# Kernel tuning notes

Measured on AMD Instinct MI355X. Metric: run time of the kernel, lower is better.

## Reference

```python
import jax, jax.numpy as jnp
import numpy as np

N_LAYERS = 4
GAMMA = 0.5
D_MODEL = 256
D_STATE = 64
D_CONV = 4
EXPAND = 2
D_INNER = EXPAND * D_MODEL            # 512 (= headdim, so nheads = 1)
NHEADS = 1
CONV_DIM = D_INNER + 2 * D_STATE      # 640
D_IN_PROJ = 2 * D_INNER + 2 * D_STATE + NHEADS  # 1153
VOCAB = 100
VOCAB_PAD = 104                        # padded to multiple of 8 by MambaConfig
BATCH = 8
SEQ = 2048


def setup_inputs() -> dict:
    key = jax.random.key(0)
    ks = jax.random.split(key, 8)
    def nrm(k, shape):
        # gamma init: std = 1 / d1**gamma, d1 = shape[0]
        return (jax.random.normal(k, shape, jnp.float32) * (1.0 / shape[0] ** GAMMA))
    inp = {}
    inp["input_ids"] = jax.random.randint(ks[0], (BATCH, SEQ), 0, VOCAB)
    inp["embed"] = nrm(ks[1], (VOCAB_PAD, D_MODEL))          # tied embedding / lm_head
    inp["in_proj_w"] = nrm(ks[2], (N_LAYERS * D_IN_PROJ, D_MODEL)).reshape(N_LAYERS, D_IN_PROJ, D_MODEL)
    inp["conv_w"] = nrm(ks[3], (N_LAYERS * CONV_DIM, D_CONV)).reshape(N_LAYERS, CONV_DIM, D_CONV)
    inp["conv_b"] = jnp.zeros((N_LAYERS, CONV_DIM), jnp.float32)
    inp["dt_bias"] = jax.random.uniform(ks[4], (N_LAYERS, NHEADS), jnp.float32, -4.0, -1.0)
    inp["A_log"] = jnp.log(jax.random.uniform(ks[5], (N_LAYERS, NHEADS), jnp.float32, 1.0, 16.0))
    inp["Dparam"] = jnp.ones((N_LAYERS, NHEADS), jnp.float32)
    inp["norm_g_w"] = jnp.ones((N_LAYERS, D_INNER), jnp.float32)
    inp["out_proj_w"] = nrm(ks[6], (N_LAYERS * D_MODEL, D_INNER)).reshape(N_LAYERS, D_MODEL, D_INNER)
    inp["block_norm_w"] = jnp.ones((N_LAYERS, D_MODEL), jnp.float32)
    inp["norm_f_w"] = jnp.ones((D_MODEL,), jnp.float32)
    return inp


def rmsnorm(x, w, eps=1e-5):
    return x * jax.lax.rsqrt(jnp.mean(x * x, axis=-1, keepdims=True) + eps) * w


def ssm_scan(x, dt, A, Bc, Cc):
    # x: (B,L,P)  dt: (B,L)  A: scalar  Bc,Cc: (B,L,N). Sequential selective scan.
    def step(h, inp):  # h: (B,P,N)
        x_t, dt_t, b_t, c_t = inp
        h = h * jnp.exp(dt_t * A)[:, None, None] + (dt_t[:, None] * x_t)[:, :, None] * b_t[:, None, :]
        y = jnp.einsum('bpn,bn->bp', h, c_t)
        return h, y
    h0 = jnp.zeros((x.shape[0], x.shape[2], Bc.shape[2]), x.dtype)
    xs = (jnp.swapaxes(x, 0, 1), jnp.swapaxes(dt, 0, 1), jnp.swapaxes(Bc, 0, 1), jnp.swapaxes(Cc, 0, 1))
    _, ys = jax.lax.scan(step, h0, xs)
    return jnp.swapaxes(ys, 0, 1)  # (B,L,P)


def mamba2_mixer(h, ipw, cw, cb, dtb, alog, dp, ngw, opw):
    zxbcdt = h @ ipw.T                                   # (B,L,1153)
    z = zxbcdt[..., :D_INNER]
    xBC = zxbcdt[..., D_INNER:D_INNER + CONV_DIM]
    dt_raw = zxbcdt[..., D_INNER + CONV_DIM:]            # (B,L,1)
    # depthwise causal conv1d (kernel D_CONV) + SiLU
    xp = jnp.pad(xBC, ((0, 0), (D_CONV - 1, 0), (0, 0)))
    L = xBC.shape[1]
    conv = sum(xp[:, k:k + L, :] * cw[:, k] for k in range(D_CONV)) + cb
    xBC = jax.nn.silu(conv)
    x = xBC[..., :D_INNER]
    Bc = xBC[..., D_INNER:D_INNER + D_STATE]
    Cc = xBC[..., D_INNER + D_STATE:]
    dt = jax.nn.softplus(dt_raw[..., 0] + dtb[0])        # (B,L), nheads=1
    A = -jnp.exp(alog[0])
    y = ssm_scan(x, dt, A, Bc, Cc) + dp[0] * x
    y = rmsnorm(y * jax.nn.silu(z), ngw)                 # RMSNormGated (norm after gate)
    return y @ opw.T


def reference(input_ids, embed, in_proj_w, conv_w, conv_b, dt_bias, A_log, Dparam,
              norm_g_w, out_proj_w, block_norm_w, norm_f_w):
    hidden = embed[input_ids]                            # (B,L,D_MODEL)
    residual = None
    for i in range(N_LAYERS):
        residual = hidden if residual is None else hidden + residual
        hidden = rmsnorm(residual, block_norm_w[i])
        hidden = mamba2_mixer(hidden, in_proj_w[i], conv_w[i], conv_b[i], dt_bias[i],
                              A_log[i], Dparam[i], norm_g_w[i], out_proj_w[i])
    residual = hidden + residual
    final = rmsnorm(residual, norm_f_w)
    logits = final @ embed.T                             # tied lm_head, (B,L,VOCAB_PAD)
    return logits[:, -1, :VOCAB]                         # last-token logits, (B,VOCAB)
```

## Files before the change

kernel.cpp:

```cpp
#include <hip/hip_runtime.h>
#include <math.h>

#define NB    8
#define LSEQ  2048
#define TKN   16384
#define DM    256
#define DI    512
#define DS    64
#define DIP   1153
#define DIPP  1160
#define CDIM  640
#define NL    4
#define NC    16
#define CL    128
#define VOC   100

typedef short bf16x8 __attribute__((ext_vector_type(8)));
typedef short bf16x4 __attribute__((ext_vector_type(4)));
typedef float f32x4  __attribute__((ext_vector_type(4)));
typedef unsigned short ushort_t;

__device__ __forceinline__ float block_reduce_sum256(float v) {
  __shared__ float sred[4];
  #pragma unroll
  for (int off = 32; off > 0; off >>= 1) v += __shfl_down(v, off, 64);
  int lane = threadIdx.x & 63, wid = threadIdx.x >> 6;
  if (lane == 0) sred[wid] = v;
  __syncthreads();
  return sred[0] + sred[1] + sred[2] + sred[3];
}

__device__ __forceinline__ unsigned short f2bf(float f) {
  unsigned int u = __float_as_uint(f);
  unsigned int r = u + 0x7FFFu + ((u >> 16) & 1u);
  return (unsigned short)(r >> 16);
}
__device__ __forceinline__ float bf2f(unsigned short u) {
  return __uint_as_float(((unsigned int)u) << 16);
}

__global__ __launch_bounds__(256) void convert_w(const float* __restrict__ ipw,
    const float* __restrict__ opw, ushort_t* __restrict__ wbi, ushort_t* __restrict__ wbo) {
  const int n1 = NL * DIP * DM;
  const int n2 = NL * DM * DI;
  int i4 = (blockIdx.x * 256 + threadIdx.x) * 4;
  if (i4 < n1) {
    float4 v = *(const float4*)(ipw + i4);
    bf16x4 o; o[0] = (short)f2bf(v.x); o[1] = (short)f2bf(v.y);
    o[2] = (short)f2bf(v.z); o[3] = (short)f2bf(v.w);
    *(bf16x4*)(wbi + i4) = o;
  } else {
    int j = i4 - n1;
    if (j < n2) {
      float4 v = *(const float4*)(opw + j);
      bf16x4 o; o[0] = (short)f2bf(v.x); o[1] = (short)f2bf(v.y);
      o[2] = (short)f2bf(v.z); o[3] = (short)f2bf(v.w);
      *(bf16x4*)(wbo + j) = o;
    }
  }
}

__global__ __launch_bounds__(256) void add_rmsnorm(float* __restrict__ resid,
    const float* __restrict__ mixo, ushort_t* __restrict__ hn, const float* __restrict__ w,
    const int* __restrict__ ids, const float* __restrict__ embed, int first) {
  int wave = threadIdx.x >> 6, lane = threadIdx.x & 63;
  int t = blockIdx.x * 4 + wave;
  size_t o = (size_t)t * DM + lane * 4;
  float4 r4;
  if (first) {
    int id = ids[t];
    r4 = *(const float4*)&embed[(size_t)id * DM + lane * 4];
  } else {
    float4 m4 = *(const float4*)&mixo[o];
    r4 = *(const float4*)&resid[o];
    r4.x += m4.x; r4.y += m4.y; r4.z += m4.z; r4.w += m4.w;
  }
  *(float4*)&resid[o] = r4;
  float ss = r4.x * r4.x + r4.y * r4.y + r4.z * r4.z + r4.w * r4.w;
  #pragma unroll
  for (int m = 32; m >= 1; m >>= 1) ss += __shfl_xor(ss, m, 64);
  float sc = rsqrtf(ss * (1.f / DM) + 1e-5f);
  float4 w4 = *(const float4*)&w[lane * 4];
  bf16x4 o4;
  o4[0] = (short)f2bf(r4.x * sc * w4.x);
  o4[1] = (short)f2bf(r4.y * sc * w4.y);
  o4[2] = (short)f2bf(r4.z * sc * w4.z);
  o4[3] = (short)f2bf(r4.w * sc * w4.w);
  *(bf16x4*)&hn[o] = o4;
}

#define LSTR  40
#define LSTR2 72
template<typename TC>
__global__ __launch_bounds__(256) void gemm_nt_bf16(const ushort_t* __restrict__ A,
    const ushort_t* __restrict__ Bw, TC* __restrict__ C, int N, int K, int ldc) {
  __shared__ short sA[128 * LSTR2];
  __shared__ short sB[128 * LSTR2];
  int tid = threadIdx.x;
  int bn = blockIdx.x * 128;
  int bm = blockIdx.y * 128;
  int wave = tid >> 6, lane = tid & 63;
  int wm = (wave >> 1) * 64, wn = (wave & 1) * 64;
  int q = lane >> 4, c = lane & 15;

  f32x4 acc[4][4];
  #pragma unroll
  for (int i = 0; i < 4; ++i)
    #pragma unroll
    for (int j = 0; j < 4; ++j) acc[i][j] = (f32x4)0.f;

  int sr = tid >> 1;
  int sc = (tid & 1) * 32;
  const ushort_t* Ag = A + (size_t)(bm + sr) * K + sc;
  const ushort_t* Bg = Bw + (size_t)(bn + sr) * K + sc;
  bool bok = (bn + sr) < N;
  short* sAp = &sA[sr * LSTR2 + sc];
  short* sBp = &sB[sr * LSTR2 + sc];

  for (int k0 = 0; k0 < K; k0 += 64) {
    bf16x8 a0 = *(const bf16x8*)(Ag + k0);
    bf16x8 a1 = *(const bf16x8*)(Ag + k0 + 8);
    bf16x8 a2 = *(const bf16x8*)(Ag + k0 + 16);
    bf16x8 a3 = *(const bf16x8*)(Ag + k0 + 24);
    bf16x8 b0 = (bf16x8)(short)0, b1 = (bf16x8)(short)0;
    bf16x8 b2 = (bf16x8)(short)0, b3 = (bf16x8)(short)0;
    if (bok) {
      b0 = *(const bf16x8*)(Bg + k0);
      b1 = *(const bf16x8*)(Bg + k0 + 8);
      b2 = *(const bf16x8*)(Bg + k0 + 16);
      b3 = *(const bf16x8*)(Bg + k0 + 24);
    }
    __syncthreads();
    *(bf16x8*)(sAp)      = a0;
    *(bf16x8*)(sAp + 8)  = a1;
    *(bf16x8*)(sAp + 16) = a2;
    *(bf16x8*)(sAp + 24) = a3;
    *(bf16x8*)(sBp)      = b0;
    *(bf16x8*)(sBp + 8)  = b1;
    *(bf16x8*)(sBp + 16) = b2;
    *(bf16x8*)(sBp + 24) = b3;
    __syncthreads();
    #pragma unroll
    for (int ks = 0; ks < 2; ++ks) {
      bf16x8 af[4], bfr[4];
      #pragma unroll
      for (int i = 0; i < 4; ++i)
        af[i] = *(const bf16x8*)&sA[(wm + i * 16 + c) * LSTR2 + ks * 32 + q * 8];
      #pragma unroll
      for (int j = 0; j < 4; ++j)
        bfr[j] = *(const bf16x8*)&sB[(wn + j * 16 + c) * LSTR2 + ks * 32 + q * 8];
      #pragma unroll
      for (int i = 0; i < 4; ++i)
        #pragma unroll
        for (int j = 0; j < 4; ++j)
          acc[i][j] = __builtin_amdgcn_mfma_f32_16x16x32_bf16(af[i], bfr[j], acc[i][j], 0, 0, 0);
    }
  }
  #pragma unroll
  for (int i = 0; i < 4; ++i) {
    int m = bm + wm + i * 16 + q * 4;
    #pragma unroll
    for (int j = 0; j < 4; ++j) {
      int n = bn + wn + j * 16 + c;
      if (n < N) {
        #pragma unroll
        for (int r = 0; r < 4; ++r) {
          if constexpr (sizeof(TC) == 2)
            C[(size_t)(m + r) * ldc + n] = (TC)f2bf(acc[i][j][r]);
          else
            C[(size_t)(m + r) * ldc + n] = acc[i][j][r];
        }
      }
    }
  }
}

__global__ __launch_bounds__(256) void outproj_fused(const ushort_t* __restrict__ yb,
    const ushort_t* __restrict__ zx, const ushort_t* __restrict__ Bw,
    const float* __restrict__ gw, float* __restrict__ Cout) {
  __shared__ short sA[64 * LSTR];
  __shared__ short sB[128 * LSTR];
  __shared__ float swl[DI];
  __shared__ float rs[256];
  int tid = threadIdx.x;
  int bn = blockIdx.x * 128;
  int bm = blockIdx.y * 64;
  int wave = tid >> 6, lane = tid & 63;
  int wm = (wave >> 1) * 32, wn = (wave & 1) * 64;
  int q = lane >> 4, c = lane & 15;
  swl[tid] = gw[tid];
  swl[tid + 256] = gw[tid + 256];

  f32x4 acc[2][4];
  #pragma unroll
  for (int i = 0; i < 2; ++i)
    #pragma unroll
    for (int j = 0; j < 4; ++j) acc[i][j] = (f32x4)0.f;

  int ar = tid >> 2, ak = (tid & 3) * 8;
  int br = tid >> 1, bk = (tid & 1) * 16;
  const ushort_t* yrow = yb + (size_t)(bm + ar) * DI + ak;
  const ushort_t* zrow = zx + (size_t)(bm + ar) * DIPP + ak;
  const ushort_t* Bg = Bw + (size_t)(bn + br) * DI + bk;
  short* sAp = &sA[ar * LSTR + ak];
  short* sBp = &sB[br * LSTR + bk];
  float sumsq = 0.f;
  __syncthreads();

  for (int k0 = 0; k0 < DI; k0 += 32) {
    bf16x8 y8 = *(const bf16x8*)(yrow + k0);
    bf16x8 z8 = *(const bf16x8*)(zrow + k0);
    bf16x8 b0 = *(const bf16x8*)(Bg + k0);
    bf16x8 b1 = *(const bf16x8*)(Bg + k0 + 8);
    bf16x8 g8;
    #pragma unroll
    for (int e = 0; e < 8; ++e) {
      float zz = bf2f((ushort_t)z8[e]);
      float gg = bf2f((ushort_t)y8[e]) * (zz / (1.f + __expf(-zz)));
      sumsq += gg * gg;
      g8[e] = (short)f2bf(gg * swl[k0 + ak + e]);
    }
    __syncthreads();
    *(bf16x8*)(sAp)     = g8;
    *(bf16x8*)(sBp)     = b0;
    *(bf16x8*)(sBp + 8) = b1;
    __syncthreads();
    bf16x8 af[2], bfr[4];
    #pragma unroll
    for (int i = 0; i < 2; ++i)
      af[i] = *(const bf16x8*)&sA[(wm + i * 16 + c) * LSTR + q * 8];
    #pragma unroll
    for (int j = 0; j < 4; ++j)
      bfr[j] = *(const bf16x8*)&sB[(wn + j * 16 + c) * LSTR + q * 8];
    #pragma unroll
    for (int i = 0; i < 2; ++i)
      #pragma unroll
      for (int j = 0; j < 4; ++j)
        acc[i][j] = __builtin_amdgcn_mfma_f32_16x16x32_bf16(af[i], bfr[j], acc[i][j], 0, 0, 0);
  }
  rs[tid] = sumsq;
  __syncthreads();
  #pragma unroll
  for (int i = 0; i < 2; ++i) {
    #pragma unroll
    for (int r = 0; r < 4; ++r) {
      int ml = wm + i * 16 + q * 4 + r;
      float rtot = rs[ml * 4] + rs[ml * 4 + 1] + rs[ml * 4 + 2] + rs[ml * 4 + 3];
      float scale = rsqrtf(rtot * (1.f / DI) + 1e-5f);
      #pragma unroll
      for (int j = 0; j < 4; ++j) {
        int n = bn + wn + j * 16 + c;
        Cout[(size_t)(bm + ml) * DM + n] = scale * acc[i][j][r];
      }
    }
  }
}

__global__ __launch_bounds__(256) void conv_silu(const ushort_t* __restrict__ zx,
    const float* __restrict__ cw, const float* __restrict__ cb,
    const float* __restrict__ dtb, ushort_t* __restrict__ xo,
    ushort_t* __restrict__ Bo, ushort_t* __restrict__ Co, ushort_t* __restrict__ Ut) {
  __shared__ ushort_t tile[67 * 128];
  __shared__ ushort_t tt[128 * 72];
  __shared__ float sdt[64];
  int tid = threadIdx.x;
  int ct = blockIdx.x, tb_ = blockIdx.y, b = blockIdx.z;
  int c0 = ct * 128, l0 = tb_ * 64;
  size_t rowb = (size_t)b * LSEQ;
  bool isx = (ct < 4);
  for (int slot = tid; slot < 67 * 16; slot += 256) {
    int r = slot >> 4, gg = slot & 15;
    int l = l0 + r - 3;
    bf16x8 v = (bf16x8)(short)0;
    if (l >= 0) v = *(const bf16x8*)&zx[(rowb + l) * DIPP + DI + c0 + gg * 8];
    *(bf16x8*)&tile[r * 128 + gg * 8] = v;
  }
  if (isx && tid < 64) sdt[tid] = dtb[rowb + l0 + tid];
  int g = tid & 15, tq = tid >> 4;
  int cbase = c0 + g * 8;
  float w[4][8], bias[8];
  #pragma unroll
  for (int e = 0; e < 8; ++e) {
    float4 wv = *(const float4*)&cw[(cbase + e) * 4];
    w[0][e] = wv.x; w[1][e] = wv.y; w[2][e] = wv.z; w[3][e] = wv.w;
    bias[e] = cb[cbase + e];
  }
  __syncthreads();
  bf16x8 rows[7];
  #pragma unroll
  for (int r = 0; r < 7; ++r)
    rows[r] = *(const bf16x8*)&tile[(tq * 4 + r) * 128 + g * 8];
  #pragma unroll
  for (int it = 0; it < 4; ++it) {
    int t = tq * 4 + it;
    size_t tl = rowb + l0 + t;
    float dtv = isx ? sdt[t] : 0.f;
    bf16x8 o;
    #pragma unroll
    for (int e = 0; e < 8; ++e) {
      float s = bias[e]
              + w[0][e] * bf2f((ushort_t)rows[it][e])
              + w[1][e] * bf2f((ushort_t)rows[it + 1][e])
              + w[2][e] * bf2f((ushort_t)rows[it + 2][e])
              + w[3][e] * bf2f((ushort_t)rows[it + 3][e]);
      float v = s / (1.f + __expf(-s));
      o[e] = (short)f2bf(v);
      if (isx) tt[(g * 8 + e) * 72 + t] = f2bf(v * dtv);
    }
    if (isx) {
      *(bf16x8*)&xo[tl * DI + cbase] = o;
    } else if (g < 8) {
      *(bf16x8*)&Bo[tl * DS + (cbase - DI)] = o;
    } else {
      *(bf16x8*)&Co[tl * DS + (cbase - DI - DS)] = o;
    }
  }
  if (isx) {
    __syncthreads();
    #pragma unroll
    for (int pass = 0; pass < 4; ++pass) {
      int slot = pass * 256 + tid;
      int op = slot >> 3, sg = slot & 7;
      bf16x8 v = *(const bf16x8*)&tt[op * 72 + sg * 8];
      *(bf16x8*)&Ut[((size_t)b * DI + c0 + op) * LSEQ + l0 + sg * 8] = v;
    }
  }
}

__global__ __launch_bounds__(256) void csum_k(const ushort_t* __restrict__ zx,
    const float* __restrict__ dtbias, float* __restrict__ dtb, float* __restrict__ csumb) {
  int tid = threadIdx.x;
  int wave = tid >> 6, lane = tid & 63;
  int cg = blockIdx.x * 4 + wave;
  int b = cg >> 4, ch = cg & 15;
  size_t base = (size_t)b * LSEQ + ch * CL;
  float bias = dtbias[0];
  float x0 = bf2f(zx[(base + 2 * lane) * DIPP + (DIP - 1)]) + bias;
  float x1 = bf2f(zx[(base + 2 * lane + 1) * DIPP + (DIP - 1)]) + bias;
  float d0 = (x0 > 20.f) ? x0 : log1pf(__expf(x0));
  float d1 = (x1 > 20.f) ? x1 : log1pf(__expf(x1));
  dtb[base + 2 * lane] = d0;
  dtb[base + 2 * lane + 1] = d1;
  float p = d0 + d1;
  #pragma unroll
  for (int off = 1; off < 64; off <<= 1) {
    float t = __shfl_up(p, off, 64);
    if (lane >= off) p += t;
  }
  csumb[base + 2 * lane]     = p - d1;
  csumb[base + 2 * lane + 1] = p;
}

__global__ __launch_bounds__(256) void state_gemm(const ushort_t* __restrict__ Bb,
    const ushort_t* __restrict__ Ut, const float* __restrict__ csumb,
    const float* __restrict__ alog, float* __restrict__ hst) {
  __shared__ short sW[64 * 144];
  __shared__ short sX[128 * 40];
  __shared__ float scs[128];
  int tid = threadIdx.x;
  int ph = blockIdx.x, ch = blockIdx.y, b = blockIdx.z;
  int bc = b * NC + ch;
  size_t tb = (size_t)b * LSEQ + ch * CL;
  float Aval = -expf(alog[0]);
  if (tid < 128) scs[tid] = csumb[tb + tid];
  __syncthreads();
  float Stot = scs[127];
  {
    int s = tid >> 1, noff = (tid & 1) * 32;
    float scale = __expf(Aval * (Stot - scs[s]));
    #pragma unroll
    for (int blk = 0; blk < 4; ++blk) {
      bf16x8 v = *(const bf16x8*)&Bb[(tb + s) * DS + noff + blk * 8];
      #pragma unroll
      for (int e = 0; e < 8; ++e)
        sW[(noff + blk * 8 + e) * 144 + s] = (short)f2bf(bf2f((ushort_t)v[e]) * scale);
    }
  }
  int wave = tid >> 6, lane = tid & 63;
  int wn = (wave >> 1) * 32, wp = (wave & 1) * 64;
  int q = lane >> 4, c = lane & 15;
  f32x4 acc[2][4];
  #pragma unroll
  for (int i = 0; i < 2; ++i)
    #pragma unroll
    for (int j = 0; j < 4; ++j) acc[i][j] = (f32x4)0.f;

  for (int ks = 0; ks < 4; ++ks) {
    __syncthreads();
    {
      int r = tid >> 1, off = (tid & 1) * 16;
      size_t ua = ((size_t)b * DI + ph * 128 + r) * LSEQ + ch * CL + ks * 32 + off;
      bf16x8 u0 = *(const bf16x8*)&Ut[ua];
      bf16x8 u1 = *(const bf16x8*)&Ut[ua + 8];
      *(bf16x8*)&sX[r * 40 + off]     = u0;
      *(bf16x8*)&sX[r * 40 + off + 8] = u1;
    }
    __syncthreads();
    bf16x8 af[2], bfr[4];
    #pragma unroll
    for (int i = 0; i < 2; ++i)
      af[i] = *(const bf16x8*)&sW[(wn + i * 16 + c) * 144 + ks * 32 + q * 8];
    #pragma unroll
    for (int j = 0; j < 4; ++j)
      bfr[j] = *(const bf16x8*)&sX[(wp + j * 16 + c) * 40 + q * 8];
    #pragma unroll
    for (int i = 0; i < 2; ++i)
      #pragma unroll
      for (int j = 0; j < 4; ++j)
        acc[i][j] = __builtin_amdgcn_mfma_f32_16x16x32_bf16(af[i], bfr[j], acc[i][j], 0, 0, 0);
  }
  #pragma unroll
  for (int i = 0; i < 2; ++i) {
    int n = wn + i * 16 + q * 4;
    #pragma unroll
    for (int j = 0; j < 4; ++j) {
      int pg = ph * 128 + wp + j * 16 + c;
      #pragma unroll
      for (int r = 0; r < 4; ++r)
        hst[((size_t)bc * DS + n + r) * DI + pg] = acc[i][j][r];
    }
  }
}

__global__ __launch_bounds__(256) void combine2(const float* __restrict__ hst,
    const float* __restrict__ csumb, const float* __restrict__ alog,
    ushort_t* __restrict__ hin) {
  __shared__ ushort_t ts[64 * 17];
  int tid = threadIdx.x;
  int pt = blockIdx.x, nt = blockIdx.y, b = blockIdx.z;
  int p0 = pt * 64, n0 = nt * 16;
  int pl = tid & 63, ng = tid >> 6;
  float Aval = -expf(alog[0]);
  float h[4];
  #pragma unroll
  for (int i = 0; i < 4; ++i) h[i] = 0.f;
  for (int c = 0; c < NC; ++c) {
    int bc = b * NC + c;
    #pragma unroll
    for (int i = 0; i < 4; ++i)
      ts[pl * 17 + ng * 4 + i] = f2bf(h[i]);
    __syncthreads();
    {
      int on = tid & 15;
      #pragma unroll
      for (int pass = 0; pass < 4; ++pass) {
        int op = (tid >> 4) + pass * 16;
        hin[((size_t)bc * DI + p0 + op) * DS + n0 + on] = ts[op * 17 + on];
      }
    }
    __syncthreads();
    float Sc = csumb[(size_t)b * LSEQ + c * CL + CL - 1];
    float dec = __expf(Aval * Sc);
    #pragma unroll
    for (int i = 0; i < 4; ++i) {
      float loc = hst[((size_t)bc * DS + n0 + ng * 4 + i) * DI + p0 + pl];
      h[i] = h[i] * dec + loc;
    }
  }
}

__global__ __launch_bounds__(256) void y_gemm(const ushort_t* __restrict__ Bb,
    const ushort_t* __restrict__ Cb, const ushort_t* __restrict__ Ut,
    const ushort_t* __restrict__ hin, const float* __restrict__ csumb,
    const float* __restrict__ alog, const float* __restrict__ dpar,
    const ushort_t* __restrict__ xb, ushort_t* __restrict__ y) {
  __shared__ short sC[128 * 72];
  __shared__ short sM[128 * 136];
  __shared__ short sU[128 * 80];
  __shared__ float scs[128];
  int tid = threadIdx.x;
  int ph = blockIdx.x, ch = blockIdx.y, b = blockIdx.z;
  int bc = b * NC + ch;
  size_t tb = (size_t)b * LSEQ + ch * CL;
  float Aval = -expf(alog[0]);
  float dp = dpar[0];
  int wave = tid >> 6, lane = tid & 63;
  int q = lane >> 4, c = lane & 15;

  {
    int r = tid >> 1, off = (tid & 1) * 32;
    #pragma unroll
    for (int blk = 0; blk < 4; ++blk) {
      *(bf16x8*)&sC[r * 72 + off + blk * 8] = *(const bf16x8*)&Cb[(tb + r) * DS + off + blk * 8];
      *(bf16x8*)&sU[r * 80 + off + blk * 8] = *(const bf16x8*)&Bb[(tb + r) * DS + off + blk * 8];
    }
  }
  if (tid < 128) scs[tid] = csumb[tb + tid];
  __syncthreads();

  {
    int wm = (wave >> 1) * 64, wss = (wave & 1) * 64;
    if (wave == 1) {
      #pragma unroll
      for (int i = 0; i < 4; ++i) {
        #pragma unroll
        for (int r = 0; r < 4; ++r) {
          int t = i * 16 + q * 4 + r;
          #pragma unroll
          for (int j = 0; j < 4; ++j)
            sM[t * 136 + 64 + j * 16 + c] = 0;
        }
      }
    } else {
      f32x4 g[4][4];
      #pragma unroll
      for (int i = 0; i < 4; ++i)
        #pragma unroll
        for (int j = 0; j < 4; ++j) g[i][j] = (f32x4)0.f;
      #pragma unroll
      for (int k0 = 0; k0 < 64; k0 += 32) {
        bf16x8 af[4], bfr[4];
        #pragma unroll
        for (int i = 0; i < 4; ++i)
          af[i] = *(const bf16x8*)&sC[(wm + i * 16 + c) * 72 + k0 + q * 8];
        #pragma unroll
        for (int j = 0; j < 4; ++j)
          bfr[j] = *(const bf16x8*)&sU[(wss + j * 16 + c) * 80 + k0 + q * 8];
        #pragma unroll
        for (int i = 0; i < 4; ++i)
          #pragma unroll
          for (int j = 0; j < 4; ++j)
            g[i][j] = __builtin_amdgcn_mfma_f32_16x16x32_bf16(af[i], bfr[j], g[i][j], 0, 0, 0);
      }
      #pragma unroll
      for (int i = 0; i < 4; ++i) {
        #pragma unroll
        for (int r = 0; r < 4; ++r) {
          int t = wm + i * 16 + q * 4 + r;
          float ct = scs[t];
          #pragma unroll
          for (int j = 0; j < 4; ++j) {
            int s = wss + j * 16 + c;
            float v = g[i][j][r];
            float m = (s <= t) ? v * __expf(Aval * (ct - scs[s])) : 0.f;
            sM[t * 136 + s] = (short)f2bf(m);
          }
        }
      }
    }
  }

  int wm2 = (wave >> 1) * 64, wp = (wave & 1) * 64;
  f32x4 acc[4][4];
  #pragma unroll
  for (int i = 0; i < 4; ++i)
    #pragma unroll
    for (int j = 0; j < 4; ++j) acc[i][j] = (f32x4)0.f;

  for (int ks = 0; ks < 4; ++ks) {
    __syncthreads();
    {
      int r = tid >> 1, off = (tid & 1) * 16;
      size_t ua = ((size_t)b * DI + ph * 128 + r) * LSEQ + ch * CL + ks * 32 + off;
      bf16x8 u0 = *(const bf16x8*)&Ut[ua];
      bf16x8 u1 = *(const bf16x8*)&Ut[ua + 8];
      *(bf16x8*)&sU[r * 40 + off]     = u0;
      *(bf16x8*)&sU[r * 40 + off + 8] = u1;
    }
    __syncthreads();
    bf16x8 af[4], bfr[4];
    #pragma unroll
    for (int i = 0; i < 4; ++i)
      af[i] = *(const bf16x8*)&sM[(wm2 + i * 16 + c) * 136 + ks * 32 + q * 8];
    #pragma unroll
    for (int j = 0; j < 4; ++j)
      bfr[j] = *(const bf16x8*)&sU[(wp + j * 16 + c) * 40 + q * 8];
    #pragma unroll
    for (int i = 0; i < 4; ++i)
      #pragma unroll
      for (int j = 0; j < 4; ++j)
        acc[i][j] = __builtin_amdgcn_mfma_f32_16x16x32_bf16(af[i], bfr[j], acc[i][j], 0, 0, 0);
  }

  __syncthreads();
  {
    int r = tid >> 1, off = (tid & 1) * 32;
    float sc_t = __expf(Aval * scs[r]);
    #pragma unroll
    for (int blk = 0; blk < 4; ++blk) {
      bf16x8 v = *(const bf16x8*)&sC[r * 72 + off + blk * 8];
      bf16x8 o;
      #pragma unroll
      for (int e = 0; e < 8; ++e)
        o[e] = (short)f2bf(bf2f((ushort_t)v[e]) * sc_t);
      *(bf16x8*)&sM[r * 80 + off + blk * 8] = o;
    }
  }
  for (int ks = 4; ks < 6; ++ks) {
    __syncthreads();
    {
      int r = tid >> 1, off = (tid & 1) * 16;
      size_t ha = ((size_t)bc * DI + ph * 128 + r) * DS + (ks - 4) * 32 + off;
      bf16x8 h0 = *(const bf16x8*)&hin[ha];
      bf16x8 h1 = *(const bf16x8*)&hin[ha + 8];
      *(bf16x8*)&sU[r * 40 + off]     = h0;
      *(bf16x8*)&sU[r * 40 + off + 8] = h1;
    }
    __syncthreads();
    bf16x8 af[4], bfr[4];
    #pragma unroll
    for (int i = 0; i < 4; ++i)
      af[i] = *(const bf16x8*)&sM[(wm2 + i * 16 + c) * 80 + (ks - 4) * 32 + q * 8];
    #pragma unroll
    for (int j = 0; j < 4; ++j)
      bfr[j] = *(const bf16x8*)&sU[(wp + j * 16 + c) * 40 + q * 8];
    #pragma unroll
    for (int i = 0; i < 4; ++i)
      #pragma unroll
      for (int j = 0; j < 4; ++j)
        acc[i][j] = __builtin_amdgcn_mfma_f32_16x16x32_bf16(af[i], bfr[j], acc[i][j], 0, 0, 0);
  }

  #pragma unroll
  for (int i = 0; i < 4; ++i) {
    #pragma unroll
    for (int r = 0; r < 4; ++r) {
      int t = wm2 + i * 16 + q * 4 + r;
      size_t row = (tb + t) * DI;
      #pragma unroll
      for (int j = 0; j < 4; ++j) {
        int pg = ph * 128 + wp + j * 16 + c;
        y[row + pg] = f2bf(acc[i][j][r] + dp * bf2f(xb[row + pg]));
      }
    }
  }
}

__global__ __launch_bounds__(256) void finalize(const float* __restrict__ resid,
    const float* __restrict__ mixo, const float* __restrict__ embed,
    const float* __restrict__ nfw, float* __restrict__ out) {
  int b = blockIdx.x, tid = threadIdx.x;
  __shared__ float fin[DM];
  size_t off = ((size_t)b * LSEQ + (LSEQ - 1)) * DM;
  float r = resid[off + tid] + mixo[off + tid];
  float ss = block_reduce_sum256(r * r);
  fin[tid] = r * rsqrtf(ss * (1.f / DM) + 1e-5f) * nfw[tid];
  __syncthreads();
  if (tid < VOC) {
    float acc = 0.f;
    #pragma unroll 8
    for (int d = 0; d < DM; ++d) acc += fin[d] * embed[(size_t)tid * DM + d];
    out[b * VOC + tid] = acc;
  }
}

extern "C" void kernel_launch(void* const* d_in, const int* in_sizes, int n_in,
                              void* d_out, int out_size, void* d_ws, size_t ws_size,
                              hipStream_t stream) {
  const int*   ids   = (const int*)d_in[0];
  const float* embed = (const float*)d_in[1];
  const float* ipw   = (const float*)d_in[2];
  const float* cw    = (const float*)d_in[3];
  const float* cb    = (const float*)d_in[4];
  const float* dtbias= (const float*)d_in[5];
  const float* alog  = (const float*)d_in[6];
  const float* dpar  = (const float*)d_in[7];
  const float* ngw   = (const float*)d_in[8];
  const float* opw   = (const float*)d_in[9];
  const float* bnw   = (const float*)d_in[10];
  const float* nfw   = (const float*)d_in[11];
  float* out = (float*)d_out;

  char* p = (char*)d_ws;
  float* resid = (float*)p;            p += (size_t)TKN * DM * 4;
  float* mixo  = (float*)p;            p += (size_t)TKN * DM * 4;
  ushort_t* hn = (ushort_t*)p;         p += (size_t)TKN * DM * 2;
  ushort_t* zx = (ushort_t*)p;         p += (size_t)TKN * DIPP * 2;
  float* dtb   = (float*)p;            p += (size_t)TKN * 4;
  float* csumb = (float*)p;            p += (size_t)TKN * 4;
  ushort_t* xb = (ushort_t*)p;         p += (size_t)TKN * DI * 2;
  ushort_t* yb = (ushort_t*)p;         p += (size_t)TKN * DI * 2;
  ushort_t* Bb = (ushort_t*)p;         p += (size_t)TKN * DS * 2;
  ushort_t* Cb = (ushort_t*)p;         p += (size_t)TKN * DS * 2;
  ushort_t* Ut = (ushort_t*)p;         p += (size_t)TKN * DI * 2;
  ushort_t* hin= (ushort_t*)p;         p += (size_t)NB * NC * DI * DS * 2;
  ushort_t* wbi= (ushort_t*)p;         p += (size_t)NL * DIP * DM * 2;
  ushort_t* wbo= (ushort_t*)p;         p += (size_t)NL * DM * DI * 2;
  float* hst = (float*)yb;

  convert_w<<<(NL * DIP * DM + NL * DM * DI + 1023) / 1024, 256, 0, stream>>>(
      ipw, opw, wbi, wbo);

  for (int i = 0; i < NL; ++i) {
    add_rmsnorm<<<TKN / 4, 256, 0, stream>>>(resid, mixo, hn, bnw + (size_t)i * DM,
                                             ids, embed, i == 0 ? 1 : 0);
    gemm_nt_bf16<ushort_t><<<dim3((DIP + 127) / 128, TKN / 128), 256, 0, stream>>>(
        hn, wbi + (size_t)i * DIP * DM, zx, DIP, DM, DIPP);
    csum_k<<<32, 256, 0, stream>>>(zx, dtbias + i, dtb, csumb);
    conv_silu<<<dim3(CDIM / 128, LSEQ / 64, NB), 256, 0, stream>>>(
        zx, cw + (size_t)i * CDIM * 4, cb + (size_t)i * CDIM, dtb, xb, Bb, Cb, Ut);
    state_gemm<<<dim3(4, NC, NB), 256, 0, stream>>>(Bb, Ut, csumb, alog + i, hst);
    combine2<<<dim3(DI / 64, 4, NB), 256, 0, stream>>>(hst, csumb, alog + i, hin);
    y_gemm<<<dim3(4, NC, NB), 256, 0, stream>>>(Bb, Cb, Ut, hin, csumb, alog + i,
                                                dpar + i, xb, yb);
    outproj_fused<<<dim3(2, TKN / 64), 256, 0, stream>>>(
        yb, zx, wbo + (size_t)i * DM * DI, ngw + (size_t)i * DI, mixo);
  }

  finalize<<<NB, 256, 0, stream>>>(resid, mixo, embed, nfw, out);
}
```

Before: 580.5 us.

## Prefetch U/h tiles into registers, pack sM stores, skip zero causal MFMAs

In state_gemm and y_gemm, the next K-slice of Ut (and later hin) is loaded into registers while the current slice is computed, so global latency overlaps the MFMA work. The bf16 writes to sM are packed into 32-bit stores by pairing lanes with a shuffle. Waves whose rows lie in the first causal half skip the MFMAs for the upper-triangular K slices, which are all zero. The cost is extra register pressure and some control-flow divergence across waves.

After: 584.6 us. Within noise of the previous version (+0.7%).

```diff
diff --git a/kernel.cpp b/kernel.cpp
--- a/kernel.cpp
+++ b/kernel.cpp
@@ -362,6 +362,10 @@
   int bc = b * NC + ch;
   size_t tb = (size_t)b * LSEQ + ch * CL;
   float Aval = -expf(alog[0]);
+  int r2 = tid >> 1, off16 = (tid & 1) * 16;
+  size_t ubase = ((size_t)b * DI + ph * 128 + r2) * LSEQ + ch * CL + off16;
+  bf16x8 pf0 = *(const bf16x8*)&Ut[ubase];
+  bf16x8 pf1 = *(const bf16x8*)&Ut[ubase + 8];
   if (tid < 128) scs[tid] = csumb[tb + tid];
   __syncthreads();
   float Stot = scs[127];
@@ -387,13 +391,11 @@
 
   for (int ks = 0; ks < 4; ++ks) {
     __syncthreads();
-    {
-      int r = tid >> 1, off = (tid & 1) * 16;
-      size_t ua = ((size_t)b * DI + ph * 128 + r) * LSEQ + ch * CL + ks * 32 + off;
-      bf16x8 u0 = *(const bf16x8*)&Ut[ua];
-      bf16x8 u1 = *(const bf16x8*)&Ut[ua + 8];
-      *(bf16x8*)&sX[r * 40 + off]     = u0;
-      *(bf16x8*)&sX[r * 40 + off + 8] = u1;
+    *(bf16x8*)&sX[r2 * 40 + off16]     = pf0;
+    *(bf16x8*)&sX[r2 * 40 + off16 + 8] = pf1;
+    if (ks < 3) {
+      pf0 = *(const bf16x8*)&Ut[ubase + (ks + 1) * 32];
+      pf1 = *(const bf16x8*)&Ut[ubase + (ks + 1) * 32 + 8];
     }
     __syncthreads();
     bf16x8 af[2], bfr[4];
@@ -477,6 +479,12 @@
   int wave = tid >> 6, lane = tid & 63;
   int q = lane >> 4, c = lane & 15;
 
+  int r2 = tid >> 1, off16 = (tid & 1) * 16;
+  size_t ubase = ((size_t)b * DI + ph * 128 + r2) * LSEQ + ch * CL + off16;
+  size_t hbase = ((size_t)bc * DI + ph * 128 + r2) * DS + off16;
+  bf16x8 pf0 = *(const bf16x8*)&Ut[ubase];
+  bf16x8 pf1 = *(const bf16x8*)&Ut[ubase + 8];
+
   {
     int r = tid >> 1, off = (tid & 1) * 32;
     #pragma unroll
@@ -496,9 +504,11 @@
         #pragma unroll
         for (int r = 0; r < 4; ++r) {
           int t = i * 16 + q * 4 + r;
-          #pragma unroll
-          for (int j = 0; j < 4; ++j)
-            sM[t * 136 + 64 + j * 16 + c] = 0;
+          if ((c & 1) == 0) {
+            #pragma unroll
+            for (int j = 0; j < 4; ++j)
+              *(unsigned int*)&sM[t * 136 + 64 + j * 16 + c] = 0u;
+          }
         }
       }
     } else {
@@ -533,7 +543,10 @@
             int s = wss + j * 16 + c;
             float v = g[i][j][r];
             float m = (s <= t) ? v * __expf(Aval * (ct - scs[s])) : 0.f;
-            sM[t * 136 + s] = (short)f2bf(m);
+            unsigned int mb = (unsigned int)f2bf(m);
+            unsigned int partner = __shfl_xor(mb, 1, 64);
+            if ((c & 1) == 0)
+              *(unsigned int*)&sM[t * 136 + s] = mb | (partner << 16);
           }
         }
       }
@@ -549,27 +562,30 @@
 
   for (int ks = 0; ks < 4; ++ks) {
     __syncthreads();
-    {
-      int r = tid >> 1, off = (tid & 1) * 16;
-      size_t ua = ((size_t)b * DI + ph * 128 + r) * LSEQ + ch * CL + ks * 32 + off;
-      bf16x8 u0 = *(const bf16x8*)&Ut[ua];
-      bf16x8 u1 = *(const bf16x8*)&Ut[ua + 8];
-      *(bf16x8*)&sU[r * 40 + off]     = u0;
-      *(bf16x8*)&sU[r * 40 + off + 8] = u1;
-    }
-    __syncthreads();
-    bf16x8 af[4], bfr[4];
-    #pragma unroll
-    for (int i = 0; i < 4; ++i)
-      af[i] = *(const bf16x8*)&sM[(wm2 + i * 16 + c) * 136 + ks * 32 + q * 8];
-    #pragma unroll
-    for (int j = 0; j < 4; ++j)
-      bfr[j] = *(const bf16x8*)&sU[(wp + j * 16 + c) * 40 + q * 8];
-    #pragma unroll
-    for (int i = 0; i < 4; ++i)
+    *(bf16x8*)&sU[r2 * 40 + off16]     = pf0;
+    *(bf16x8*)&sU[r2 * 40 + off16 + 8] = pf1;
+    if (ks < 3) {
+      pf0 = *(const bf16x8*)&Ut[ubase + (ks + 1) * 32];
+      pf1 = *(const bf16x8*)&Ut[ubase + (ks + 1) * 32 + 8];
+    } else {
+      pf0 = *(const bf16x8*)&hin[hbase];
+      pf1 = *(const bf16x8*)&hin[hbase + 8];
+    }
+    __syncthreads();
+    if (!(wm2 == 0 && ks >= 2)) {
+      bf16x8 af[4], bfr[4];
+      #pragma unroll
+      for (int i = 0; i < 4; ++i)
+        af[i] = *(const bf16x8*)&sM[(wm2 + i * 16 + c) * 136 + ks * 32 + q * 8];
       #pragma unroll
       for (int j = 0; j < 4; ++j)
-        acc[i][j] = __builtin_amdgcn_mfma_f32_16x16x32_bf16(af[i], bfr[j], acc[i][j], 0, 0, 0);
+        bfr[j] = *(const bf16x8*)&sU[(wp + j * 16 + c) * 40 + q * 8];
+      #pragma unroll
+      for (int i = 0; i < 4; ++i)
+        #pragma unroll
+        for (int j = 0; j < 4; ++j)
+          acc[i][j] = __builtin_amdgcn_mfma_f32_16x16x32_bf16(af[i], bfr[j], acc[i][j], 0, 0, 0);
+    }
   }
 
   __syncthreads();
@@ -588,13 +604,11 @@
   }
   for (int ks = 4; ks < 6; ++ks) {
     __syncthreads();
-    {
-      int r = tid >> 1, off = (tid & 1) * 16;
-      size_t ha = ((size_t)bc * DI + ph * 128 + r) * DS + (ks - 4) * 32 + off;
-      bf16x8 h0 = *(const bf16x8*)&hin[ha];
-      bf16x8 h1 = *(const bf16x8*)&hin[ha + 8];
-      *(bf16x8*)&sU[r * 40 + off]     = h0;
-      *(bf16x8*)&sU[r * 40 + off + 8] = h1;
+    *(bf16x8*)&sU[r2 * 40 + off16]     = pf0;
+    *(bf16x8*)&sU[r2 * 40 + off16 + 8] = pf1;
+    if (ks == 4) {
+      pf0 = *(const bf16x8*)&hin[hbase + 32];
+      pf1 = *(const bf16x8*)&hin[hbase + 32 + 8];
     }
     __syncthreads();
     bf16x8 af[4], bfr[4];
```

## Load MFMA operands directly from global memory and drop LDS staging in SSM chunk GEMMs

Applied to the files above, without the earlier changes.

In state_gemm and y_gemm, the U, B, C and h operand fragments are now read straight from global memory into MFMA registers instead of being staged through shared memory. This removes most __syncthreads barriers and LDS traffic. The C scaling is applied in registers, and the causal y GEMM skips the K-steps that are fully masked for the upper row half. The M-matrix stores are packed into 32-bit writes via a lane shuffle. The trade-off is more uncoalesced, redundant global and L2 reads per wave in exchange for lower LDS use and fewer barriers, which may also raise occupancy.

New measurement: 601.6 us. +3.6%, slower.

```diff
diff --git a/kernel.cpp b/kernel.cpp
--- a/kernel.cpp
+++ b/kernel.cpp
@@ -355,7 +355,6 @@
     const ushort_t* __restrict__ Ut, const float* __restrict__ csumb,
     const float* __restrict__ alog, float* __restrict__ hst) {
   __shared__ short sW[64 * 144];
-  __shared__ short sX[128 * 40];
   __shared__ float scs[128];
   int tid = threadIdx.x;
   int ph = blockIdx.x, ch = blockIdx.y, b = blockIdx.z;
@@ -376,6 +375,7 @@
         sW[(noff + blk * 8 + e) * 144 + s] = (short)f2bf(bf2f((ushort_t)v[e]) * scale);
     }
   }
+  __syncthreads();
   int wave = tid >> 6, lane = tid & 63;
   int wn = (wave >> 1) * 32, wp = (wave & 1) * 64;
   int q = lane >> 4, c = lane & 15;
@@ -385,24 +385,16 @@
     #pragma unroll
     for (int j = 0; j < 4; ++j) acc[i][j] = (f32x4)0.f;
 
+  size_t urow = (size_t)b * DI + ph * 128;
+  #pragma unroll
   for (int ks = 0; ks < 4; ++ks) {
-    __syncthreads();
-    {
-      int r = tid >> 1, off = (tid & 1) * 16;
-      size_t ua = ((size_t)b * DI + ph * 128 + r) * LSEQ + ch * CL + ks * 32 + off;
-      bf16x8 u0 = *(const bf16x8*)&Ut[ua];
-      bf16x8 u1 = *(const bf16x8*)&Ut[ua + 8];
-      *(bf16x8*)&sX[r * 40 + off]     = u0;
-      *(bf16x8*)&sX[r * 40 + off + 8] = u1;
-    }
-    __syncthreads();
     bf16x8 af[2], bfr[4];
+    #pragma unroll
+    for (int j = 0; j < 4; ++j)
+      bfr[j] = *(const bf16x8*)&Ut[(urow + wp + j * 16 + c) * LSEQ + ch * CL + ks * 32 + q * 8];
     #pragma unroll
     for (int i = 0; i < 2; ++i)
       af[i] = *(const bf16x8*)&sW[(wn + i * 16 + c) * 144 + ks * 32 + q * 8];
-    #pragma unroll
-    for (int j = 0; j < 4; ++j)
-      bfr[j] = *(const bf16x8*)&sX[(wp + j * 16 + c) * 40 + q * 8];
     #pragma unroll
     for (int i = 0; i < 2; ++i)
       #pragma unroll
@@ -464,9 +456,7 @@
     const ushort_t* __restrict__ hin, const float* __restrict__ csumb,
     const float* __restrict__ alog, const float* __restrict__ dpar,
     const ushort_t* __restrict__ xb, ushort_t* __restrict__ y) {
-  __shared__ short sC[128 * 72];
   __shared__ short sM[128 * 136];
-  __shared__ short sU[128 * 80];
   __shared__ float scs[128];
   int tid = threadIdx.x;
   int ph = blockIdx.x, ch = blockIdx.y, b = blockIdx.z;
@@ -477,14 +467,6 @@
   int wave = tid >> 6, lane = tid & 63;
   int q = lane >> 4, c = lane & 15;
 
-  {
-    int r = tid >> 1, off = (tid & 1) * 32;
-    #pragma unroll
-    for (int blk = 0; blk < 4; ++blk) {
-      *(bf16x8*)&sC[r * 72 + off + blk * 8] = *(const bf16x8*)&Cb[(tb + r) * DS + off + blk * 8];
-      *(bf16x8*)&sU[r * 80 + off + blk * 8] = *(const bf16x8*)&Bb[(tb + r) * DS + off + blk * 8];
-    }
-  }
   if (tid < 128) scs[tid] = csumb[tb + tid];
   __syncthreads();
 
@@ -492,14 +474,11 @@
     int wm = (wave >> 1) * 64, wss = (wave & 1) * 64;
     if (wave == 1) {
       #pragma unroll
-      for (int i = 0; i < 4; ++i) {
-        #pragma unroll
-        for (int r = 0; r < 4; ++r) {
-          int t = i * 16 + q * 4 + r;
-          #pragma unroll
-          for (int j = 0; j < 4; ++j)
-            sM[t * 136 + 64 + j * 16 + c] = 0;
-        }
+      for (int it = 0; it < 32; ++it) {
+        int idx = it * 64 + lane;
+        int row = idx >> 5;
+        int col = (idx & 31) * 2;
+        *(unsigned int*)&sM[row * 136 + 64 + col] = 0u;
       }
     } else {
       f32x4 g[4][4];
@@ -512,10 +491,10 @@
         bf16x8 af[4], bfr[4];
         #pragma unroll
         for (int i = 0; i < 4; ++i)
-          af[i] = *(const bf16x8*)&sC[(wm + i * 16 + c) * 72 + k0 + q * 8];
+          af[i] = *(const bf16x8*)&Cb[(tb + wm + i * 16 + c) * DS + k0 + q * 8];
         #pragma unroll
         for (int j = 0; j < 4; ++j)
-          bfr[j] = *(const bf16x8*)&sU[(wss + j * 16 + c) * 80 + k0 + q * 8];
+          bfr[j] = *(const bf16x8*)&Bb[(tb + wss + j * 16 + c) * DS + k0 + q * 8];
         #pragma unroll
         for (int i = 0; i < 4; ++i)
           #pragma unroll
@@ -533,12 +512,16 @@
             int s = wss + j * 16 + c;
             float v = g[i][j][r];
             float m = (s <= t) ? v * __expf(Aval * (ct - scs[s])) : 0.f;
-            sM[t * 136 + s] = (short)f2bf(m);
+            unsigned int mb = (unsigned int)f2bf(m);
+            unsigned int partner = __shfl_xor(mb, 1, 64);
+            if ((c & 1) == 0)
+              *(unsigned int*)&sM[t * 136 + s] = mb | (partner << 16);
           }
         }
       }
     }
   }
+  __syncthreads();
 
   int wm2 = (wave >> 1) * 64, wp = (wave & 1) * 64;
   f32x4 acc[4][4];
@@ -547,63 +530,42 @@
     #pragma unroll
     for (int j = 0; j < 4; ++j) acc[i][j] = (f32x4)0.f;
 
+  size_t urow = (size_t)b * DI + ph * 128;
+  #pragma unroll
   for (int ks = 0; ks < 4; ++ks) {
-    __syncthreads();
-    {
-      int r = tid >> 1, off = (tid & 1) * 16;
-      size_t ua = ((size_t)b * DI + ph * 128 + r) * LSEQ + ch * CL + ks * 32 + off;
-      bf16x8 u0 = *(const bf16x8*)&Ut[ua];
-      bf16x8 u1 = *(const bf16x8*)&Ut[ua + 8];
-      *(bf16x8*)&sU[r * 40 + off]     = u0;
-      *(bf16x8*)&sU[r * 40 + off + 8] = u1;
-    }
-    __syncthreads();
+    if (wm2 == 0 && ks >= 2) continue;
     bf16x8 af[4], bfr[4];
+    #pragma unroll
+    for (int j = 0; j < 4; ++j)
+      bfr[j] = *(const bf16x8*)&Ut[(urow + wp + j * 16 + c) * LSEQ + ch * CL + ks * 32 + q * 8];
     #pragma unroll
     for (int i = 0; i < 4; ++i)
       af[i] = *(const bf16x8*)&sM[(wm2 + i * 16 + c) * 136 + ks * 32 + q * 8];
     #pragma unroll
-    for (int j = 0; j < 4; ++j)
-      bfr[j] = *(const bf16x8*)&sU[(wp + j * 16 + c) * 40 + q * 8];
-    #pragma unroll
     for (int i = 0; i < 4; ++i)
       #pragma unroll
       for (int j = 0; j < 4; ++j)
         acc[i][j] = __builtin_amdgcn_mfma_f32_16x16x32_bf16(af[i], bfr[j], acc[i][j], 0, 0, 0);
   }
 
-  __syncthreads();
-  {
-    int r = tid >> 1, off = (tid & 1) * 32;
-    float sc_t = __expf(Aval * scs[r]);
-    #pragma unroll
-    for (int blk = 0; blk < 4; ++blk) {
-      bf16x8 v = *(const bf16x8*)&sC[r * 72 + off + blk * 8];
-      bf16x8 o;
+  float rscale[4];
+  #pragma unroll
+  for (int i = 0; i < 4; ++i)
+    rscale[i] = __expf(Aval * scs[wm2 + i * 16 + c]);
+  size_t hrow = (size_t)bc * DI + ph * 128;
+  #pragma unroll
+  for (int ks2 = 0; ks2 < 2; ++ks2) {
+    bf16x8 af[4], bfr[4];
+    #pragma unroll
+    for (int j = 0; j < 4; ++j)
+      bfr[j] = *(const bf16x8*)&hin[(hrow + wp + j * 16 + c) * DS + ks2 * 32 + q * 8];
+    #pragma unroll
+    for (int i = 0; i < 4; ++i) {
+      bf16x8 cf = *(const bf16x8*)&Cb[(tb + wm2 + i * 16 + c) * DS + ks2 * 32 + q * 8];
       #pragma unroll
       for (int e = 0; e < 8; ++e)
-        o[e] = (short)f2bf(bf2f((ushort_t)v[e]) * sc_t);
-      *(bf16x8*)&sM[r * 80 + off + blk * 8] = o;
-    }
-  }
-  for (int ks = 4; ks < 6; ++ks) {
-    __syncthreads();
-    {
-      int r = tid >> 1, off = (tid & 1) * 16;
-      size_t ha = ((size_t)bc * DI + ph * 128 + r) * DS + (ks - 4) * 32 + off;
-      bf16x8 h0 = *(const bf16x8*)&hin[ha];
-      bf16x8 h1 = *(const bf16x8*)&hin[ha + 8];
-      *(bf16x8*)&sU[r * 40 + off]     = h0;
-      *(bf16x8*)&sU[r * 40 + off + 8] = h1;
-    }
-    __syncthreads();
-    bf16x8 af[4], bfr[4];
-    #pragma unroll
-    for (int i = 0; i < 4; ++i)
-      af[i] = *(const bf16x8*)&sM[(wm2 + i * 16 + c) * 80 + (ks - 4) * 32 + q * 8];
-    #pragma unroll
-    for (int j = 0; j < 4; ++j)
-      bfr[j] = *(const bf16x8*)&sU[(wp + j * 16 + c) * 40 + q * 8];
+        af[i][e] = (short)f2bf(bf2f((ushort_t)cf[e]) * rscale[i]);
+    }
     #pragma unroll
     for (int i = 0; i < 4; ++i)
       #pragma unroll
```

## Fuse residual add and next-layer RMSNorm into out-projection epilogue

Applied to the files above, without the earlier changes.

The out-projection kernel now computes full 256-wide output rows per block (32 rows × 256 cols), so it can add the result into the residual stream and apply the next layer's RMSNorm in its epilogue, writing bf16 normalized activations directly. This removes the separate add_rmsnorm kernel per layer and the mixo intermediate buffer round trip. The final norm is folded in the same way, so finalize just reads the bf16 hn. Separately, y_gemm skips MFMA work for causally-masked upper-triangle chunks when wm2==0 and ks>=2. The trade-off is fewer blocks per launch with larger B tiles, and final logits now come from bf16-rounded activations.

New measurement: 562.5 us. 3.1% less time.

```diff
diff --git a/kernel.cpp b/kernel.cpp
--- a/kernel.cpp
+++ b/kernel.cpp
@@ -60,21 +60,14 @@
   }
 }
 
-__global__ __launch_bounds__(256) void add_rmsnorm(float* __restrict__ resid,
-    const float* __restrict__ mixo, ushort_t* __restrict__ hn, const float* __restrict__ w,
-    const int* __restrict__ ids, const float* __restrict__ embed, int first) {
+__global__ __launch_bounds__(256) void embed_rmsnorm(float* __restrict__ resid,
+    ushort_t* __restrict__ hn, const float* __restrict__ w,
+    const int* __restrict__ ids, const float* __restrict__ embed) {
   int wave = threadIdx.x >> 6, lane = threadIdx.x & 63;
   int t = blockIdx.x * 4 + wave;
   size_t o = (size_t)t * DM + lane * 4;
-  float4 r4;
-  if (first) {
-    int id = ids[t];
-    r4 = *(const float4*)&embed[(size_t)id * DM + lane * 4];
-  } else {
-    float4 m4 = *(const float4*)&mixo[o];
-    r4 = *(const float4*)&resid[o];
-    r4.x += m4.x; r4.y += m4.y; r4.z += m4.z; r4.w += m4.w;
-  }
+  int id = ids[t];
+  float4 r4 = *(const float4*)&embed[(size_t)id * DM + lane * 4];
   *(float4*)&resid[o] = r4;
   float ss = r4.x * r4.x + r4.y * r4.y + r4.z * r4.z + r4.w * r4.w;
   #pragma unroll
@@ -91,9 +84,8 @@
 
 #define LSTR  40
 #define LSTR2 72
-template<typename TC>
 __global__ __launch_bounds__(256) void gemm_nt_bf16(const ushort_t* __restrict__ A,
-    const ushort_t* __restrict__ Bw, TC* __restrict__ C, int N, int K, int ldc) {
+    const ushort_t* __restrict__ Bw, ushort_t* __restrict__ C, int N, int K, int ldc) {
   __shared__ short sA[128 * LSTR2];
   __shared__ short sB[128 * LSTR2];
   int tid = threadIdx.x;
@@ -164,94 +156,116 @@
       int n = bn + wn + j * 16 + c;
       if (n < N) {
         #pragma unroll
-        for (int r = 0; r < 4; ++r) {
-          if constexpr (sizeof(TC) == 2)
-            C[(size_t)(m + r) * ldc + n] = (TC)f2bf(acc[i][j][r]);
-          else
-            C[(size_t)(m + r) * ldc + n] = acc[i][j][r];
-        }
+        for (int r = 0; r < 4; ++r)
+          C[(size_t)(m + r) * ldc + n] = f2bf(acc[i][j][r]);
       }
     }
   }
 }
 
-__global__ __launch_bounds__(256) void outproj_fused(const ushort_t* __restrict__ yb,
+__global__ __launch_bounds__(256) void outproj_norm(const ushort_t* __restrict__ yb,
     const ushort_t* __restrict__ zx, const ushort_t* __restrict__ Bw,
-    const float* __restrict__ gw, float* __restrict__ Cout) {
-  __shared__ short sA[64 * LSTR];
-  __shared__ short sB[128 * LSTR];
+    const float* __restrict__ gw, float* __restrict__ resid,
+    const float* __restrict__ wnext, ushort_t* __restrict__ hn) {
+  __shared__ short sA[32 * LSTR];
+  __shared__ short sB[256 * LSTR];
   __shared__ float swl[DI];
-  __shared__ float rs[256];
+  __shared__ float swn[DM];
+  __shared__ float rs[128];
+  __shared__ float rs2[32 * 2];
   int tid = threadIdx.x;
-  int bn = blockIdx.x * 128;
-  int bm = blockIdx.y * 64;
+  int bm = blockIdx.x * 32;
   int wave = tid >> 6, lane = tid & 63;
-  int wm = (wave >> 1) * 32, wn = (wave & 1) * 64;
+  int wm = (wave >> 1) * 16, wn = (wave & 1) * 128;
   int q = lane >> 4, c = lane & 15;
   swl[tid] = gw[tid];
   swl[tid + 256] = gw[tid + 256];
-
-  f32x4 acc[2][4];
-  #pragma unroll
-  for (int i = 0; i < 2; ++i)
-    #pragma unroll
-    for (int j = 0; j < 4; ++j) acc[i][j] = (f32x4)0.f;
+  swn[tid] = wnext[tid];
+
+  f32x4 acc[8];
+  #pragma unroll
+  for (int j = 0; j < 8; ++j) acc[j] = (f32x4)0.f;
 
   int ar = tid >> 2, ak = (tid & 3) * 8;
-  int br = tid >> 1, bk = (tid & 1) * 16;
+  bool isa = tid < 128;
   const ushort_t* yrow = yb + (size_t)(bm + ar) * DI + ak;
   const ushort_t* zrow = zx + (size_t)(bm + ar) * DIPP + ak;
-  const ushort_t* Bg = Bw + (size_t)(bn + br) * DI + bk;
-  short* sAp = &sA[ar * LSTR + ak];
-  short* sBp = &sB[br * LSTR + bk];
+  const ushort_t* Bg = Bw + (size_t)tid * DI;
   float sumsq = 0.f;
   __syncthreads();
 
   for (int k0 = 0; k0 < DI; k0 += 32) {
-    bf16x8 y8 = *(const bf16x8*)(yrow + k0);
-    bf16x8 z8 = *(const bf16x8*)(zrow + k0);
+    bf16x8 g8;
+    if (isa) {
+      bf16x8 y8 = *(const bf16x8*)(yrow + k0);
+      bf16x8 z8 = *(const bf16x8*)(zrow + k0);
+      #pragma unroll
+      for (int e = 0; e < 8; ++e) {
+        float zz = bf2f((ushort_t)z8[e]);
+        float gg = bf2f((ushort_t)y8[e]) * (zz / (1.f + __expf(-zz)));
+        sumsq += gg * gg;
+        g8[e] = (short)f2bf(gg * swl[k0 + ak + e]);
+      }
+    }
     bf16x8 b0 = *(const bf16x8*)(Bg + k0);
     bf16x8 b1 = *(const bf16x8*)(Bg + k0 + 8);
-    bf16x8 g8;
-    #pragma unroll
-    for (int e = 0; e < 8; ++e) {
-      float zz = bf2f((ushort_t)z8[e]);
-      float gg = bf2f((ushort_t)y8[e]) * (zz / (1.f + __expf(-zz)));
-      sumsq += gg * gg;
-      g8[e] = (short)f2bf(gg * swl[k0 + ak + e]);
-    }
-    __syncthreads();
-    *(bf16x8*)(sAp)     = g8;
-    *(bf16x8*)(sBp)     = b0;
-    *(bf16x8*)(sBp + 8) = b1;
-    __syncthreads();
-    bf16x8 af[2], bfr[4];
-    #pragma unroll
-    for (int i = 0; i < 2; ++i)
-      af[i] = *(const bf16x8*)&sA[(wm + i * 16 + c) * LSTR + q * 8];
-    #pragma unroll
-    for (int j = 0; j < 4; ++j)
-      bfr[j] = *(const bf16x8*)&sB[(wn + j * 16 + c) * LSTR + q * 8];
-    #pragma unroll
-    for (int i = 0; i < 2; ++i)
-      #pragma unroll
-      for (int j = 0; j < 4; ++j)
-        acc[i][j] = __builtin_amdgcn_mfma_f32_16x16x32_bf16(af[i], bfr[j], acc[i][j], 0, 0, 0);
-  }
-  rs[tid] = sumsq;
-  __syncthreads();
-  #pragma unroll
-  for (int i = 0; i < 2; ++i) {
-    #pragma unroll
-    for (int r = 0; r < 4; ++r) {
-      int ml = wm + i * 16 + q * 4 + r;
-      float rtot = rs[ml * 4] + rs[ml * 4 + 1] + rs[ml * 4 + 2] + rs[ml * 4 + 3];
-      float scale = rsqrtf(rtot * (1.f / DI) + 1e-5f);
-      #pragma unroll
-      for (int j = 0; j < 4; ++j) {
-        int n = bn + wn + j * 16 + c;
-        Cout[(size_t)(bm + ml) * DM + n] = scale * acc[i][j][r];
-      }
+    bf16x8 b2 = *(const bf16x8*)(Bg + k0 + 16);
+    bf16x8 b3 = *(const bf16x8*)(Bg + k0 + 24);
+    __syncthreads();
+    if (isa) *(bf16x8*)&sA[ar * LSTR + ak] = g8;
+    *(bf16x8*)&sB[tid * LSTR]      = b0;
+    *(bf16x8*)&sB[tid * LSTR + 8]  = b1;
+    *(bf16x8*)&sB[tid * LSTR + 16] = b2;
+    *(bf16x8*)&sB[tid * LSTR + 24] = b3;
+    __syncthreads();
+    bf16x8 af = *(const bf16x8*)&sA[(wm + c) * LSTR + q * 8];
+    #pragma unroll
+    for (int j = 0; j < 8; ++j) {
+      bf16x8 bfr = *(const bf16x8*)&sB[(wn + j * 16 + c) * LSTR + q * 8];
+      acc[j] = __builtin_amdgcn_mfma_f32_16x16x32_bf16(af, bfr, acc[j], 0, 0, 0);
+    }
+  }
+  if (isa) rs[tid] = sumsq;
+  __syncthreads();
+
+  float outv[8][4];
+  float sq2[4];
+  #pragma unroll
+  for (int r = 0; r < 4; ++r) {
+    int row = wm + q * 4 + r;
+    float s1 = rsqrtf((rs[row * 4] + rs[row * 4 + 1] + rs[row * 4 + 2] + rs[row * 4 + 3])
+                      * (1.f / DI) + 1e-5f);
+    float sq = 0.f;
+    #pragma unroll
+    for (int j = 0; j < 8; ++j) {
+      int col = wn + j * 16 + c;
+      size_t ro = (size_t)(bm + row) * DM + col;
+      float rn = resid[ro] + s1 * acc[j][r];
+      resid[ro] = rn;
+      outv[j][r] = rn;
+      sq += rn * rn;
+    }
+    sq2[r] = sq;
+  }
+  #pragma unroll
+  for (int r = 0; r < 4; ++r) {
+    #pragma unroll
+    for (int m = 1; m <= 8; m <<= 1) sq2[r] += __shfl_xor(sq2[r], m, 64);
+  }
+  if (c == 0) {
+    #pragma unroll
+    for (int r = 0; r < 4; ++r)
+      rs2[(wm + q * 4 + r) * 2 + (wave & 1)] = sq2[r];
+  }
+  __syncthreads();
+  #pragma unroll
+  for (int r = 0; r < 4; ++r) {
+    int row = wm + q * 4 + r;
+    float s2 = rsqrtf((rs2[row * 2] + rs2[row * 2 + 1]) * (1.f / DM) + 1e-5f);
+    #pragma unroll
+    for (int j = 0; j < 8; ++j) {
+      int col = wn + j * 16 + c;
+      hn[(size_t)(bm + row) * DM + col] = f2bf(outv[j][r] * s2 * swn[col]);
     }
   }
 }
@@ -558,18 +572,20 @@
       *(bf16x8*)&sU[r * 40 + off + 8] = u1;
     }
     __syncthreads();
-    bf16x8 af[4], bfr[4];
-    #pragma unroll
-    for (int i = 0; i < 4; ++i)
-      af[i] = *(const bf16x8*)&sM[(wm2 + i * 16 + c) * 136 + ks * 32 + q * 8];
-    #pragma unroll
-    for (int j = 0; j < 4; ++j)
-      bfr[j] = *(const bf16x8*)&sU[(wp + j * 16 + c) * 40 + q * 8];
-    #pragma unroll
-    for (int i = 0; i < 4; ++i)
+    if (!(wm2 == 0 && ks >= 2)) {
+      bf16x8 af[4], bfr[4];
+      #pragma unroll
+      for (int i = 0; i < 4; ++i)
+        af[i] = *(const bf16x8*)&sM[(wm2 + i * 16 + c) * 136 + ks * 32 + q * 8];
       #pragma unroll
       for (int j = 0; j < 4; ++j)
-        acc[i][j] = __builtin_amdgcn_mfma_f32_16x16x32_bf16(af[i], bfr[j], acc[i][j], 0, 0, 0);
+        bfr[j] = *(const bf16x8*)&sU[(wp + j * 16 + c) * 40 + q * 8];
+      #pragma unroll
+      for (int i = 0; i < 4; ++i)
+        #pragma unroll
+        for (int j = 0; j < 4; ++j)
+          acc[i][j] = __builtin_amdgcn_mfma_f32_16x16x32_bf16(af[i], bfr[j], acc[i][j], 0, 0, 0);
+    }
   }
 
   __syncthreads();
@@ -626,15 +642,12 @@
   }
 }
 
-__global__ __launch_bounds__(256) void finalize(const float* __restrict__ resid,
-    const float* __restrict__ mixo, const float* __restrict__ embed,
-    const float* __restrict__ nfw, float* __restrict__ out) {
+__global__ __launch_bounds__(256) void finalize(const ushort_t* __restrict__ hn,
+    const float* __restrict__ embed, float* __restrict__ out) {
   int b = blockIdx.x, tid = threadIdx.x;
   __shared__ float fin[DM];
   size_t off = ((size_t)b * LSEQ + (LSEQ - 1)) * DM;
-  float r = resid[off + tid] + mixo[off + tid];
-  float ss = block_reduce_sum256(r * r);
-  fin[tid] = r * rsqrtf(ss * (1.f / DM) + 1e-5f) * nfw[tid];
+  fin[tid] = bf2f(hn[off + tid]);
   __syncthreads();
   if (tid < VOC) {
     float acc = 0.f;
@@ -663,7 +676,6 @@
 
   char* p = (char*)d_ws;
   float* resid = (float*)p;            p += (size_t)TKN * DM * 4;
-  float* mixo  = (float*)p;            p += (size_t)TKN * DM * 4;
   ushort_t* hn = (ushort_t*)p;         p += (size_t)TKN * DM * 2;
   ushort_t* zx = (ushort_t*)p;         p += (size_t)TKN * DIPP * 2;
   float* dtb   = (float*)p;            p += (size_t)TKN * 4;
@@ -680,11 +692,10 @@
 
   convert_w<<<(NL * DIP * DM + NL * DM * DI + 1023) / 1024, 256, 0, stream>>>(
       ipw, opw, wbi, wbo);
+  embed_rmsnorm<<<TKN / 4, 256, 0, stream>>>(resid, hn, bnw, ids, embed);
 
   for (int i = 0; i < NL; ++i) {
-    add_rmsnorm<<<TKN / 4, 256, 0, stream>>>(resid, mixo, hn, bnw + (size_t)i * DM,
-                                             ids, embed, i == 0 ? 1 : 0);
-    gemm_nt_bf16<ushort_t><<<dim3((DIP + 127) / 128, TKN / 128), 256, 0, stream>>>(
+    gemm_nt_bf16<<<dim3((DIP + 127) / 128, TKN / 128), 256, 0, stream>>>(
         hn, wbi + (size_t)i * DIP * DM, zx, DIP, DM, DIPP);
     csum_k<<<32, 256, 0, stream>>>(zx, dtbias + i, dtb, csumb);
     conv_silu<<<dim3(CDIM / 128, LSEQ / 64, NB), 256, 0, stream>>>(
@@ -693,9 +704,10 @@
     combine2<<<dim3(DI / 64, 4, NB), 256, 0, stream>>>(hst, csumb, alog + i, hin);
     y_gemm<<<dim3(4, NC, NB), 256, 0, stream>>>(Bb, Cb, Ut, hin, csumb, alog + i,
                                                 dpar + i, xb, yb);
-    outproj_fused<<<dim3(2, TKN / 64), 256, 0, stream>>>(
-        yb, zx, wbo + (size_t)i * DM * DI, ngw + (size_t)i * DI, mixo);
-  }
-
-  finalize<<<NB, 256, 0, stream>>>(resid, mixo, embed, nfw, out);
-}
+    const float* wnext = (i < NL - 1) ? (bnw + (size_t)(i + 1) * DM) : nfw;
+    outproj_norm<<<TKN / 32, 256, 0, stream>>>(
+        yb, zx, wbo + (size_t)i * DM * DI, ngw + (size_t)i * DI, resid, wnext, hn);
+  }
+
+  finalize<<<NB, 256, 0, stream>>>(hn, embed, out);
+}
```
